# Kernel tuning notes

Measured on AMD Instinct MI355X. Metric: run time of the kernel, lower is better.

## Reference

```python
import jax, jax.numpy as jnp
import numpy as np

B, C = 2, 2
D = H = W = 192
N_BIF = 64                 # bif ids 0..63; labels = bif*4 + stub (stub in 1..3)
NUM_LABELS = 4 * N_BIF     # 256
MIN_STUBS = 2
MIN_VOXELS = 1
TEMP = 0.2


def setup_inputs() -> dict:
    key = jax.random.key(0)
    k1, k2 = jax.random.split(key)
    pred = jax.random.normal(k1, (B, C, D, H, W), dtype=jnp.float32)
    stub_label_map = jax.random.randint(k2, (B, 1, D, H, W), 0, NUM_LABELS).astype(jnp.float32)
    return {"pred": pred, "stub_label_map": stub_label_map}


def reference(pred, stub_label_map):
    # foreground probability: softmax over channel dim, take class 1
    fg = jax.nn.softmax(pred, axis=1)[:, 1]                     # [B,D,H,W]
    labels = jnp.round(stub_label_map[:, 0]).astype(jnp.int32)  # [B,D,H,W]

    Bn = fg.shape[0]
    fg_flat = fg.reshape(Bn, -1)
    lab_flat = labels.reshape(Bn, -1)

    seg = lambda v, i: jax.ops.segment_sum(v, i, num_segments=NUM_LABELS)
    sums = jax.vmap(seg)(fg_flat, lab_flat)                      # [B, NUM_LABELS]
    counts = jax.vmap(seg)(jnp.ones_like(fg_flat), lab_flat)     # [B, NUM_LABELS]

    # group labels as [bif, stub]; drop bif 0 and stub 0 (never used in loop)
    sums = sums.reshape(Bn, N_BIF, 4)[:, 1:, 1:4]                # [B, N_BIF-1, 3]
    counts = counts.reshape(Bn, N_BIF, 4)[:, 1:, 1:4]

    valid = counts >= MIN_VOXELS                                 # stub has enough voxels
    means = sums / jnp.maximum(counts, 1.0)                      # per-stub mean fg prob

    # softmin over the valid stubs of each bif (masked softmax of -mean/temp)
    logits = jnp.where(valid, -means / TEMP, -1e9)
    weights = jax.nn.softmax(logits, axis=-1)
    score = jnp.sum(jnp.where(valid, means * weights, 0.0), axis=-1)  # [B, N_BIF-1]

    valid_bif = jnp.sum(valid, axis=-1) >= MIN_STUBS
    total = jnp.sum(jnp.where(valid_bif, 1.0 - score, 0.0))
    n_bifs = jnp.sum(valid_bif)
    return jnp.where(n_bifs > 0, total / jnp.maximum(n_bifs, 1).astype(total.dtype), 0.0)
```

## Files before the change

### kernel.cpp

```cpp
#include <hip/hip_runtime.h>
#include <math.h>

#define BATCH     2
#define NLAB      256
#define VOX       (192*192*192)
#define TEMP      0.2f
#define GRIDX     768
#define NITER     ((VOX/4)/(GRIDX*256))
#define NPART     16

#define STEP      4096.0f
#define INV_STEP  (1.0f/4096.0f)

typedef unsigned int u32;
typedef __attribute__((ext_vector_type(8))) short bf16x8;
typedef __attribute__((ext_vector_type(4))) float f32x4;
union FragU { uint4 u; bf16x8 v; };

__device__ __forceinline__ u32 fgbf16(float pa, float pc) {
    const float fg = __builtin_amdgcn_rcpf(1.0f + __expf(pa - pc));
    u32 bits = __float_as_uint(fg);
    bits += 0x7FFFu + ((bits >> 16) & 1u);
    return bits >> 16;
}

__device__ __forceinline__ void voxmask(float pl, u32& hm, u32& lmm) {
    const u32 lab = ((u32)(int)(pl + 0.5f)) & 255u;
    hm  = 1u << (lab >> 4);
    lmm = 1u << (lab & 15u);
}

#define PAIRH(whi, wlo, fp, aw, b1w, b2w) do {                              \
    const u32 _h = ((whi) >> mlane) & 0x10001u;                             \
    const u32 _l = ((wlo) >> mlane) & 0x10001u;                             \
    aw  = __umul24(_h, 0x3F80u);                                            \
    b1w = __umul24(_l, 0x3F80u);                                            \
    b2w = (fp) & __umul24(_l, 0xFFFFu);                                     \
} while (0)

__global__ __launch_bounds__(256) void histo_kernel(
    const float* __restrict__ pred,
    const float* __restrict__ labmap,
    float* __restrict__ ws_slots)
{
    __shared__ __align__(16) u32 s_iv[4][2][256];
    __shared__ __align__(16) u32 s_fg[4][2][128];

    const int b    = blockIdx.y;
    const int tid  = threadIdx.x;
    const int w    = tid >> 6;
    const int lane = tid & 63;
    const u32 mlane = (u32)(lane & 15);
    const int g    = lane >> 4;

    const float4* p0 = (const float4*)(pred + (size_t)b * 2 * VOX);
    const float4* p1 = (const float4*)(pred + (size_t)b * 2 * VOX + VOX);
    const float4* lm = (const float4*)(labmap + (size_t)b * VOX);

    f32x4 accC = {0.f, 0.f, 0.f, 0.f};
    f32x4 accS = {0.f, 0.f, 0.f, 0.f};

    const int base = blockIdx.x * 256 + tid;

    float4 a = p0[base];
    float4 c = p1[base];
    float4 l = lm[base];

    for (int it = 0; it < NITER; ++it) {
        const int nit = (it + 1 < NITER) ? (it + 1) : it;
        const int inx = base + nit * (GRIDX * 256);
        const float4 an = p0[inx];
        const float4 cn = p1[inx];
        const float4 ln = lm[inx];

        u32 hm0, lm0, hm1, lm1, hm2, lm2, hm3, lm3;
        voxmask(l.x, hm0, lm0);
        voxmask(l.y, hm1, lm1);
        voxmask(l.z, hm2, lm2);
        voxmask(l.w, hm3, lm3);
        const u32 whiA = hm0 | (hm1 << 16);
        const u32 wloA = lm0 | (lm1 << 16);
        const u32 whiB = hm2 | (hm3 << 16);
        const u32 wloB = lm2 | (lm3 << 16);
        const u32 fgA  = fgbf16(a.x, c.x) | (fgbf16(a.y, c.y) << 16);
        const u32 fgB  = fgbf16(a.z, c.z) | (fgbf16(a.w, c.w) << 16);

        u32* iv  = &s_iv[w][it & 1][0];
        u32* fgp = &s_fg[w][it & 1][0];
        *(uint4*)(iv + (lane << 2)) = make_uint4(whiA, wloA, whiB, wloB);
        *(uint2*)(fgp + (lane << 1)) = make_uint2(fgA, fgB);

        const u32* rp = iv + (g << 3);
        const u32* rf = fgp + (g << 2);
        #pragma unroll
        for (int t = 0; t < 8; ++t) {
            const uint4 q0 = *(const uint4*)(rp + t * 32);
            const uint4 q1 = *(const uint4*)(rp + t * 32 + 4);
            const uint4 fq = *(const uint4*)(rf + t * 16);
            u32 a0, a1, a2, a3, b10, b11, b12, b13, b20, b21, b22, b23;
            PAIRH(q0.x, q0.y, fq.x, a0, b10, b20);
            PAIRH(q0.z, q0.w, fq.y, a1, b11, b21);
            PAIRH(q1.x, q1.y, fq.z, a2, b12, b22);
            PAIRH(q1.z, q1.w, fq.w, a3, b13, b23);
            FragU A, B1, B2;
            A.u  = make_uint4(a0, a1, a2, a3);
            B1.u = make_uint4(b10, b11, b12, b13);
            B2.u = make_uint4(b20, b21, b22, b23);
            accC = __builtin_amdgcn_mfma_f32_16x16x32_bf16(A.v, B1.v, accC, 0, 0, 0);
            accS = __builtin_amdgcn_mfma_f32_16x16x32_bf16(A.v, B2.v, accS, 0, 0, 0);
        }

        a = an; c = cn; l = ln;
    }

    float* cnt_w = (float*)&s_iv[w][0][0];
    float* sum_w = (float*)&s_iv[w][1][0];
    const int row0 = (lane >> 4) << 2;
    const int colb = lane & 15;
    #pragma unroll
    for (int j = 0; j < 4; ++j) {
        cnt_w[(row0 + j) * 16 + colb] = accC[j];
        sum_w[(row0 + j) * 16 + colb] = accS[j];
    }
    __syncthreads();

    float cs = 0.0f, ss = 0.0f;
    #pragma unroll
    for (int ww = 0; ww < 4; ++ww) {
        cs += ((float*)&s_iv[ww][0][0])[tid];
        ss += ((float*)&s_iv[ww][1][0])[tid];
    }
    ws_slots[((size_t)(b * GRIDX + blockIdx.x)) * NLAB + tid] = ss + STEP * cs;
}

__global__ __launch_bounds__(256) void reduce_kernel(
    const float* __restrict__ ws_slots,
    float* __restrict__ psum,
    float* __restrict__ pcnt)
{
    const int bin  = threadIdx.x;
    const int b    = blockIdx.x / NPART;
    const int part = blockIdx.x % NPART;
    const int per  = GRIDX / NPART;

    float cs = 0.0f, ss = 0.0f;
    for (int s = part * per; s < (part + 1) * per; ++s) {
        float v = ws_slots[((size_t)(b * GRIDX + s)) * NLAB + bin];
        float c = floorf(v * INV_STEP + 0.5f);
        cs += c;
        ss += v - c * STEP;
    }
    psum[(size_t)blockIdx.x * NLAB + bin] = ss;
    pcnt[(size_t)blockIdx.x * NLAB + bin] = cs;
}

__global__ __launch_bounds__(256) void scalar_kernel(
    const float* __restrict__ psum,
    const float* __restrict__ pcnt,
    float* __restrict__ out)
{
    __shared__ float s_fsum[BATCH][NLAB];
    __shared__ float s_fcnt[BATCH][NLAB];

    const int tid = threadIdx.x;

    for (int b = 0; b < BATCH; ++b) {
        float ss = 0.0f, cs = 0.0f;
        for (int p = 0; p < NPART; ++p) {
            ss += psum[(size_t)(b * NPART + p) * NLAB + tid];
            cs += pcnt[(size_t)(b * NPART + p) * NLAB + tid];
        }
        s_fsum[b][tid] = ss;
        s_fcnt[b][tid] = cs;
    }
    __syncthreads();

    if (tid < 64) {
        float total = 0.0f;
        float nbifs = 0.0f;
        if (tid >= 1) {
            for (int bb = 0; bb < BATCH; ++bb) {
                float means[3];
                bool  valid[3];
                int   nvalid = 0;
                for (int s = 0; s < 3; ++s) {
                    int lab = tid * 4 + 1 + s;
                    float cnt = s_fcnt[bb][lab];
                    float sum = s_fsum[bb][lab];
                    valid[s] = (cnt >= 1.0f);
                    means[s] = sum / fmaxf(cnt, 1.0f);
                    nvalid  += valid[s] ? 1 : 0;
                }
                float logits[3], m = -3e38f;
                for (int s = 0; s < 3; ++s) {
                    logits[s] = valid[s] ? (-means[s] / TEMP) : -1e9f;
                    m = fmaxf(m, logits[s]);
                }
                float e[3], se = 0.0f;
                for (int s = 0; s < 3; ++s) { e[s] = __expf(logits[s] - m); se += e[s]; }
                float score = 0.0f;
                for (int s = 0; s < 3; ++s) {
                    if (valid[s]) score += means[s] * (e[s] / se);
                }
                if (nvalid >= 2) {
                    total += 1.0f - score;
                    nbifs += 1.0f;
                }
            }
        }
        for (int off = 32; off > 0; off >>= 1) {
            total += __shfl_down(total, off);
            nbifs += __shfl_down(nbifs, off);
        }
        if (tid == 0) {
            out[0] = (nbifs > 0.0f) ? (total / fmaxf(nbifs, 1.0f)) : 0.0f;
        }
    }
}

extern "C" void kernel_launch(void* const* d_in, const int* in_sizes, int n_in,
                              void* d_out, int out_size, void* d_ws, size_t ws_size,
                              hipStream_t stream) {
    const float* pred = (const float*)d_in[0];
    const float* lab  = (const float*)d_in[1];

    float* ws_slots = (float*)d_ws;
    float* psum = ws_slots + (size_t)BATCH * GRIDX * NLAB;
    float* pcnt = psum + (size_t)BATCH * NPART * NLAB;

    dim3 grid(GRIDX, BATCH);
    histo_kernel<<<grid, 256, 0, stream>>>(pred, lab, ws_slots);
    reduce_kernel<<<BATCH * NPART, 256, 0, stream>>>(ws_slots, psum, pcnt);
    scalar_kernel<<<1, 256, 0, stream>>>(psum, pcnt, (float*)d_out);
}
```

Before: 209.1 us.

## Deepen software pipeline in histogram kernel and set occupancy hint

The histogram loop is restructured so the label/probability packing for iteration it+1 is written to the LDS double buffer while the MFMA loop consumes iteration it, and global loads run two iterations ahead. The inner MFMA loop also prefetches the next LDS fragments one step early, and launch bounds now request 6 blocks per SM. The goal is to overlap the expf/packing ALU work and the LDS latency with the matrix ops, at the cost of more live registers. Cross-wave sync is not needed because each wave uses its own buffer slice.

```diff
diff --git a/kernel.cpp b/kernel.cpp
--- a/kernel.cpp
+++ b/kernel.cpp
@@ -7,6 +7,7 @@
 #define TEMP      0.2f
 #define GRIDX     768
 #define NITER     ((VOX/4)/(GRIDX*256))
+#define STRIDE    (GRIDX*256)
 #define NPART     16
 
 #define STEP      4096.0f
@@ -38,7 +39,21 @@
     b2w = (fp) & __umul24(_l, 0xFFFFu);                                     \
 } while (0)
 
-__global__ __launch_bounds__(256) void histo_kernel(
+#define PACKIT(av, cv, lv, WHIA, WLOA, WHIB, WLOB, FGA, FGB) do {           \
+    u32 hm0, lm0, hm1, lm1, hm2, lm2, hm3, lm3;                             \
+    voxmask((lv).x, hm0, lm0);                                              \
+    voxmask((lv).y, hm1, lm1);                                              \
+    voxmask((lv).z, hm2, lm2);                                              \
+    voxmask((lv).w, hm3, lm3);                                              \
+    WHIA = hm0 | (hm1 << 16);                                               \
+    WLOA = lm0 | (lm1 << 16);                                               \
+    WHIB = hm2 | (hm3 << 16);                                               \
+    WLOB = lm2 | (lm3 << 16);                                               \
+    FGA  = fgbf16((av).x, (cv).x) | (fgbf16((av).y, (cv).y) << 16);         \
+    FGB  = fgbf16((av).z, (cv).z) | (fgbf16((av).w, (cv).w) << 16);         \
+} while (0)
+
+__global__ __launch_bounds__(256, 6) void histo_kernel(
     const float* __restrict__ pred,
     const float* __restrict__ labmap,
     float* __restrict__ ws_slots)
@@ -62,55 +77,58 @@
 
     const int base = blockIdx.x * 256 + tid;
 
-    float4 a = p0[base];
-    float4 c = p1[base];
-    float4 l = lm[base];
+    {
+        const float4 a0 = p0[base], c0 = p1[base], l0 = lm[base];
+        u32 whiA, wloA, whiB, wloB, fgA, fgB;
+        PACKIT(a0, c0, l0, whiA, wloA, whiB, wloB, fgA, fgB);
+        *(uint4*)(&s_iv[w][0][0] + (lane << 2)) =
+            make_uint4(whiA, wloA, whiB, wloB);
+        *(uint2*)(&s_fg[w][0][0] + (lane << 1)) = make_uint2(fgA, fgB);
+    }
+    float4 a1 = p0[base + STRIDE], c1 = p1[base + STRIDE], l1 = lm[base + STRIDE];
 
     for (int it = 0; it < NITER; ++it) {
-        const int nit = (it + 1 < NITER) ? (it + 1) : it;
-        const int inx = base + nit * (GRIDX * 256);
-        const float4 an = p0[inx];
-        const float4 cn = p1[inx];
-        const float4 ln = lm[inx];
-
-        u32 hm0, lm0, hm1, lm1, hm2, lm2, hm3, lm3;
-        voxmask(l.x, hm0, lm0);
-        voxmask(l.y, hm1, lm1);
-        voxmask(l.z, hm2, lm2);
-        voxmask(l.w, hm3, lm3);
-        const u32 whiA = hm0 | (hm1 << 16);
-        const u32 wloA = lm0 | (lm1 << 16);
-        const u32 whiB = hm2 | (hm3 << 16);
-        const u32 wloB = lm2 | (lm3 << 16);
-        const u32 fgA  = fgbf16(a.x, c.x) | (fgbf16(a.y, c.y) << 16);
-        const u32 fgB  = fgbf16(a.z, c.z) | (fgbf16(a.w, c.w) << 16);
-
-        u32* iv  = &s_iv[w][it & 1][0];
-        u32* fgp = &s_fg[w][it & 1][0];
-        *(uint4*)(iv + (lane << 2)) = make_uint4(whiA, wloA, whiB, wloB);
-        *(uint2*)(fgp + (lane << 1)) = make_uint2(fgA, fgB);
-
-        const u32* rp = iv + (g << 3);
-        const u32* rf = fgp + (g << 2);
+        if (it + 1 < NITER) {
+            u32 whiA, wloA, whiB, wloB, fgA, fgB;
+            PACKIT(a1, c1, l1, whiA, wloA, whiB, wloB, fgA, fgB);
+            u32* iv  = &s_iv[w][(it + 1) & 1][0];
+            u32* fgp = &s_fg[w][(it + 1) & 1][0];
+            *(uint4*)(iv + (lane << 2)) = make_uint4(whiA, wloA, whiB, wloB);
+            *(uint2*)(fgp + (lane << 1)) = make_uint2(fgA, fgB);
+        }
+        {
+            const int nit = (it + 2 < NITER) ? (it + 2) : (NITER - 1);
+            const int inx = base + nit * STRIDE;
+            a1 = p0[inx]; c1 = p1[inx]; l1 = lm[inx];
+        }
+
+        const u32* rp = &s_iv[w][it & 1][0] + (g << 3);
+        const u32* rf = &s_fg[w][it & 1][0] + (g << 2);
+
+        uint4 q0 = *(const uint4*)(rp);
+        uint4 q1 = *(const uint4*)(rp + 4);
+        uint4 fq = *(const uint4*)(rf);
         #pragma unroll
         for (int t = 0; t < 8; ++t) {
-            const uint4 q0 = *(const uint4*)(rp + t * 32);
-            const uint4 q1 = *(const uint4*)(rp + t * 32 + 4);
-            const uint4 fq = *(const uint4*)(rf + t * 16);
-            u32 a0, a1, a2, a3, b10, b11, b12, b13, b20, b21, b22, b23;
-            PAIRH(q0.x, q0.y, fq.x, a0, b10, b20);
-            PAIRH(q0.z, q0.w, fq.y, a1, b11, b21);
-            PAIRH(q1.x, q1.y, fq.z, a2, b12, b22);
-            PAIRH(q1.z, q1.w, fq.w, a3, b13, b23);
+            uint4 q0n, q1n, fqn;
+            if (t < 7) {
+                q0n = *(const uint4*)(rp + (t + 1) * 32);
+                q1n = *(const uint4*)(rp + (t + 1) * 32 + 4);
+                fqn = *(const uint4*)(rf + (t + 1) * 16);
+            }
+            u32 a0, a1w, a2, a3, b10, b11, b12, b13, b20, b21, b22, b23;
+            PAIRH(q0.x, q0.y, fq.x, a0,  b10, b20);
+            PAIRH(q0.z, q0.w, fq.y, a1w, b11, b21);
+            PAIRH(q1.x, q1.y, fq.z, a2,  b12, b22);
+            PAIRH(q1.z, q1.w, fq.w, a3,  b13, b23);
             FragU A, B1, B2;
-            A.u  = make_uint4(a0, a1, a2, a3);
+            A.u  = make_uint4(a0, a1w, a2, a3);
             B1.u = make_uint4(b10, b11, b12, b13);
             B2.u = make_uint4(b20, b21, b22, b23);
             accC = __builtin_amdgcn_mfma_f32_16x16x32_bf16(A.v, B1.v, accC, 0, 0, 0);
             accS = __builtin_amdgcn_mfma_f32_16x16x32_bf16(A.v, B2.v, accS, 0, 0, 0);
-        }
-
-        a = an; c = cn; l = ln;
+            if (t < 7) { q0 = q0n; q1 = q1n; fq = fqn; }
+        }
     }
 
     float* cnt_w = (float*)&s_iv[w][0][0];
```

Measured after the change: 212.6 us. Within noise of the previous version (+1.6%).
